# Kernel tuning notes

Measured on AMD Instinct MI355X. Metric: run time of the kernel, lower is better.

## Reference

```python
import jax, jax.numpy as jnp
import numpy as np

# Model dims (match init_kwargs / input_specs)
L = 2      # layer_dim
B = 64     # batch
T = 512    # max seq len
D = 256    # input_dim (== hidden_dim, required by stacked wiring)
H = 256    # hidden_dim
O = 2      # output_dim


def setup_inputs() -> dict:
    key = jax.random.key(0)
    ks = jax.random.split(key, 10)
    s = 1.0 / np.sqrt(H)
    f32 = jnp.float32
    return {
        "x_data": jax.random.normal(ks[0], (B, T, D), f32),
        "x_length": jax.random.randint(ks[1], (B,), 1, T + 1),
        "x_label": jax.random.uniform(ks[2], (B,), f32),
        # Per-layer GRU-cell weights, stacked over layers (bias=False).
        "Wz": (jax.random.normal(ks[3], (L, D, H), f32) * s),
        "Uz": (jax.random.normal(ks[4], (L, H, H), f32) * s),
        "Wr": (jax.random.normal(ks[5], (L, D, H), f32) * s),
        "Ur": (jax.random.normal(ks[6], (L, H, H), f32) * s),
        "Wh": (jax.random.normal(ks[7], (L, D, H), f32) * s),
        "Uh": (jax.random.normal(ks[8], (L, H, H), f32) * s),
        # Output projection of the last layer (only last layer's `out` is used).
        "Wo": (jax.random.normal(ks[9], (H, O), f32) * s),
    }


def reference(x_data, x_length, x_label, Wz, Uz, Wr, Ur, Wh, Uh, Wo):
    # Training-mode forward: sum over batch and valid timesteps of
    # (label - sigmoid(out[:, 1]))**2, with per-layer states S1, S2
    # carried across time. Vectorized over batch; lax.scan over time.
    Tn = x_data.shape[1]
    xs = jnp.swapaxes(x_data, 0, 1)  # [T, B, D]
    S1_0 = jnp.zeros((L, B, H), x_data.dtype)
    S2_0 = jnp.zeros((L, B, H), x_data.dtype)

    def step(carry, xt):
        S1, S2 = carry
        inp = xt  # [B, D]
        for l in range(L):  # small fixed layer loop
            z = jax.nn.sigmoid(inp @ Wz[l] + S1[l] @ Uz[l])
            r = jax.nn.sigmoid(inp @ Wr[l] + S1[l] @ Ur[l])
            h = jnp.tanh(inp @ Wh[l] + (r * S1[l]) @ Uh[l])
            hn = (1.0 - z) * S1[l] + z * h          # new hidden (S1)
            S2n = z * S2[l] + (1.0 - z) * h          # secondary memory (S2)
            S1 = S1.at[l].set(hn)
            S2 = S2.at[l].set(S2n)
            inp = hn
        score = jax.nn.sigmoid((inp @ Wo)[:, 1])     # out[:, 1] -> [B]
        return (S1, S2), score

    _, scores = jax.lax.scan(step, (S1_0, S2_0), xs)  # [T, B]
    mask = (jnp.arange(Tn)[:, None] < x_length[None, :]).astype(scores.dtype)
    loss = jnp.sum(mask * (x_label[None, :] - scores) ** 2)
    return loss
```

## Files before the change

kernel.cpp:

```cpp
#include <hip/hip_runtime.h>

#define LAY 2
#define BATCH 64
#define TMAX 512
#define DIM 256
#define AST 264
#define CHUNK 16

typedef float floatx4 __attribute__((ext_vector_type(4)));
typedef __bf16 bf16x8 __attribute__((ext_vector_type(8)));
#define MFMA_FP8  __builtin_amdgcn_mfma_f32_16x16x32_fp8_fp8
#define MFMA_BF16 __builtin_amdgcn_mfma_f32_16x16x32_bf16

#define BAR_LDS() asm volatile("s_waitcnt lgkmcnt(0)\n\ts_barrier" ::: "memory")

#define OFF_WPW 0x60000
#define OFF_FLG 0x150000
#define OFF_XP  0x200000
#define OFF_HP  0x1C00000
#define OFF_HN  0x3600000

__device__ __forceinline__ unsigned short f2bf(float f) {
    unsigned int u = __float_as_uint(f);
    unsigned int r = u + 0x7fffu + ((u >> 16) & 1u);
    return (unsigned short)(r >> 16);
}
__device__ __forceinline__ unsigned int pk2(float a, float b) {
    return (unsigned int)__builtin_amdgcn_cvt_pk_fp8_f32(a, b, 0, false);
}
__device__ __forceinline__ unsigned char f2q(float a) { return (unsigned char)(pk2(a, a) & 0xff); }
__device__ __forceinline__ void unp4(unsigned int u, float* f) {
    auto lo = __builtin_amdgcn_cvt_pk_f32_fp8((int)u, false);
    auto hi = __builtin_amdgcn_cvt_pk_f32_fp8((int)u, true);
    f[0] = lo[0]; f[1] = lo[1]; f[2] = hi[0]; f[3] = hi[1];
}
__device__ __forceinline__ float sigf(float x) {
    return __builtin_amdgcn_rcpf(1.f + __expf(-x));
}
__device__ __forceinline__ float tanhfast2y(float twoy) { return 2.f * sigf(twoy) - 1.f; }

__global__ void prep_weights(const float* __restrict__ Wz, const float* __restrict__ Wr,
                             const float* __restrict__ Wh, const float* __restrict__ Uz,
                             const float* __restrict__ Ur, const float* __restrict__ Uh,
                             unsigned char* __restrict__ ws, float* __restrict__ out) {
    int T = blockIdx.x * 256 + threadIdx.x;
    if (T == 0) out[0] = 0.f;
    if (T < 192) ((int*)(ws + OFF_FLG))[T] = 0;
    if (T < 196608) {
        int e = T & 3, half = (T >> 2) & 1, lane = (T >> 3) & 63;
        int kp = (T >> 9) & 3, nt = (T >> 11) & 15, mu = T >> 15;
        int g = mu % 3, l = mu / 3;
        const float* s = (g == 0 ? Uz : g == 1 ? Ur : Uh) + l * 65536;
        int n  = nt * 16 + (lane & 15);
        int k0 = (2 * kp + half) * 32 + (lane >> 4) * 8 + 2 * e;
        float w0 = s[(k0 << 8) + n] * 8.f;
        float w1 = s[((k0 + 1) << 8) + n] * 8.f;
        int addr = ((mu * 16 + nt) * 4 + kp) * 1024 + lane * 16 + half * 8 + 2 * e;
        *(unsigned short*)(ws + addr) = (unsigned short)(pk2(w0, w1) & 0xffff);
    } else {
        int T2 = T - 196608;
        int e = T2 & 3, lane = (T2 >> 2) & 63;
        int kf = (T2 >> 8) & 7, nt = (T2 >> 11) & 15, mw = T2 >> 15;
        int g = mw % 3, l = mw / 3;
        const float* s = (g == 0 ? Wz : g == 1 ? Wr : Wh) + l * 65536;
        int n  = nt * 16 + (lane & 15);
        int k0 = kf * 32 + (lane >> 4) * 8 + 2 * e;
        unsigned int v = (unsigned int)f2bf(s[(k0 << 8) + n]) |
                         ((unsigned int)f2bf(s[((k0 + 1) << 8) + n]) << 16);
        int addr = ((mw * 16 + nt) * 8 + kf) * 1024 + lane * 16 + 4 * e;
        *(unsigned int*)(ws + OFF_WPW + addr) = v;
    }
}

template <int SCORE, int WMODE, int POST>
__device__ __forceinline__ void scan_body(
    const unsigned int* __restrict__ xp, const unsigned char* __restrict__ wpU,
    int lbase, int bg, unsigned short* __restrict__ hnout,
    const int* __restrict__ xlen, const float* __restrict__ xlab,
    const float* __restrict__ Wo, float* __restrict__ out,
    int* wflags, int* pflag,
    unsigned char (*s1q)[AST], unsigned char (*rsq)[AST], float (*s1o)[264],
    float* wo1s, int* s_rdy, int tmax)
{
    const int tid = threadIdx.x, wave = tid >> 6, lane = tid & 63;
    const int l15 = lane & 15, quad = lane >> 4;
    const int b0 = bg * 16;

    for (int i = tid; i < 16 * AST; i += 1024) ((unsigned char*)s1q)[i] = 0;
    if (SCORE && tid < DIM) wo1s[tid] = Wo[2 * tid + 1];
    const int lenr = xlen[b0 + l15];
    const float labr = SCORE ? xlab[b0 + l15] : 0.f;
    (void)lenr; (void)labr;

    const int nt = wave;
    const int colA = nt * 16 + l15, rowb = quad * 4;

    long uz[8], ur[8], uh[8];
    {
        const unsigned char* pz = wpU + (size_t)(((lbase + 0) * 16 + nt) * 4) * 1024 + lane * 16;
        const unsigned char* pr = wpU + (size_t)(((lbase + 1) * 16 + nt) * 4) * 1024 + lane * 16;
        const unsigned char* ph = wpU + (size_t)(((lbase + 2) * 16 + nt) * 4) * 1024 + lane * 16;
#pragma unroll
        for (int kf = 0; kf < 8; ++kf) {
            int o = (kf >> 1) * 1024 + (kf & 1) * 8;
            uz[kf] = *(const long*)(pz + o);
            ur[kf] = *(const long*)(pr + o);
            uh[kf] = *(const long*)(ph + o);
        }
    }
    float s1r[4] = {};
    float accl = 0.f;
    int ready = 0;
    __syncthreads();

    for (int t = 0; t < tmax; ++t) {
        if constexpr (WMODE == 1) {
            if (t >= ready) {
                if (tid == 0) {
                    int vv, g = 0;
                    for (;;) {
                        vv = 1 << 30;
#pragma unroll
                        for (int q = 0; q < 4; ++q) {
                            int m = __hip_atomic_load(wflags + q, __ATOMIC_RELAXED, __HIP_MEMORY_SCOPE_AGENT);
                            vv = m < vv ? m : vv;
                        }
                        if (vv > t || ++g > (1 << 19)) break;
                        __builtin_amdgcn_s_sleep(2);
                    }
                    __threadfence();
                    *s_rdy = vv > t ? vv : t + 1;
                }
                __syncthreads();
                ready = *s_rdy;
            }
        } else if constexpr (WMODE == 2) {
            if (t >= ready) {
                if (tid == 0) {
                    const int ch = t >> 4;
                    int g = 0;
                    for (;;) {
                        int c = __hip_atomic_load(wflags + ch, __ATOMIC_RELAXED, __HIP_MEMORY_SCOPE_AGENT);
                        if (c >= 16 || ++g > (1 << 19)) break;
                        __builtin_amdgcn_s_sleep(2);
                    }
                    __threadfence();
                    *s_rdy = (ch + 1) * CHUNK;
                }
                __syncthreads();
                ready = *s_rdy;
            }
        }

        const unsigned int* xpt = xp + (size_t)(bg * 512 + t) * 3072 + lane;
        unsigned int xz = xpt[nt * 64];
        unsigned int xr = xpt[1024 + nt * 64];
        unsigned int xh = xpt[2048 + nt * 64];

        long sf[8];
#pragma unroll
        for (int kf = 0; kf < 8; ++kf) sf[kf] = *(const long*)&s1q[l15][kf * 32 + quad * 8];
        floatx4 za = {0.f, 0.f, 0.f, 0.f}, ra = za;
#pragma unroll
        for (int kf = 0; kf < 8; ++kf) {
            ra = MFMA_FP8(sf[kf], ur[kf], ra, 0, 0, 0);
            za = MFMA_FP8(sf[kf], uz[kf], za, 0, 0, 0);
        }
        float xrf[4];
        unp4(xr, xrf);
#pragma unroll
        for (int i = 0; i < 4; ++i) {
            float r = sigf(0.125f * ra[i] + 0.0625f * xrf[i]);
            rsq[rowb + i][colA] = f2q(r * s1r[i]);
        }
        BAR_LDS();

        long rf[8];
#pragma unroll
        for (int kf = 0; kf < 8; ++kf) rf[kf] = *(const long*)&rsq[l15][kf * 32 + quad * 8];
        floatx4 ha = {0.f, 0.f, 0.f, 0.f};
#pragma unroll
        for (int kf = 0; kf < 8; ++kf) ha = MFMA_FP8(rf[kf], uh[kf], ha, 0, 0, 0);
        float xzf[4], xhf[4];
        unp4(xz, xzf); unp4(xh, xhf);
#pragma unroll
        for (int i = 0; i < 4; ++i) {
            float z = sigf(0.125f * za[i] + 0.0625f * xzf[i]);
            float h = tanhfast2y(0.25f * ha[i] + 0.125f * xhf[i]);
            float hn = (1.f - z) * s1r[i] + z * h;
            s1r[i] = hn;
            s1q[rowb + i][colA] = f2q(hn);
            s1o[rowb + i][colA] = hn;
        }
        BAR_LDS();

        if (!SCORE) {
            const int r = tid >> 6, c = (tid & 63) * 4;
            float4 f0 = *(const float4*)&s1o[r][c];
            uint2 o2;
            o2.x = f2bf(f0.x) | ((unsigned)f2bf(f0.y) << 16);
            o2.y = f2bf(f0.z) | ((unsigned)f2bf(f0.w) << 16);
            *(uint2*)(hnout + ((size_t)(b0 + r) * 512 + t) * 256 + c) = o2;
        } else if (wave == 0) {
            const int row = l15, c0 = quad * 64;
            float p = 0.f;
#pragma unroll
            for (int u = 0; u < 64; u += 4) {
                float4 sv = *(const float4*)&s1o[row][c0 + u];
                float4 wv = *(const float4*)&wo1s[c0 + u];
                p = fmaf(sv.x, wv.x, p); p = fmaf(sv.y, wv.y, p);
                p = fmaf(sv.z, wv.z, p); p = fmaf(sv.w, wv.w, p);
            }
            p += __shfl_xor(p, 16);
            p += __shfl_xor(p, 32);
            if (lane < 16 && t < lenr) {
                float sc = sigf(p);
                float d = labr - sc;
                accl = fmaf(d, d, accl);
            }
        }

        if (POST && (((t & (CHUNK - 1)) == (CHUNK - 1)) || t == tmax - 1)) {
            __syncthreads();
            if (tid == 0) {
                __threadfence();
                __hip_atomic_store(pflag, t + 1, __ATOMIC_RELEASE, __HIP_MEMORY_SCOPE_AGENT);
            }
        }
    }

    if (SCORE && wave == 0) {
        accl += __shfl_xor(accl, 1);
        accl += __shfl_xor(accl, 2);
        accl += __shfl_xor(accl, 4);
        accl += __shfl_xor(accl, 8);
        if (lane == 0) atomicAdd(out, accl);
    }
}

__global__ __launch_bounds__(1024, 4) void fused_pipeline(
    const float* __restrict__ x,
    unsigned int* __restrict__ XP, unsigned int* __restrict__ HP,
    const unsigned char* __restrict__ wpU, const unsigned char* __restrict__ wpW,
    unsigned short* __restrict__ HN,
    const int* __restrict__ xlen, const float* __restrict__ xlab,
    const float* __restrict__ Wo, float* __restrict__ out, int* flags)
{
    __shared__ __align__(16) unsigned char s1q[16][AST];
    __shared__ __align__(16) unsigned char rsq[16][AST];
    __shared__ __align__(16) float s1o[16][264];
    __shared__ float wo1s[DIM];
    __shared__ int s_rdy;

    const int bid = blockIdx.x;
    const int tid = threadIdx.x, wave = tid >> 6, lane = tid & 63;
    const int l15 = lane & 15, quad = lane >> 4;
    int* cnt = flags + 32;

    if (bid >= 24) {
        const int idx = bid - 24;
        const int pt = idx & 511, pbg = idx >> 9;
        const float* s = x + ((size_t)(pbg * 16 + l15) * 512 + pt) * 256;
        bf16x8 af[8];
#pragma unroll
        for (int kf = 0; kf < 8; ++kf) {
            float4 a = *(const float4*)(s + kf * 32 + quad * 8);
            float4 b = *(const float4*)(s + kf * 32 + quad * 8 + 4);
            union { unsigned short u[8]; bf16x8 v; } cv;
            cv.u[0] = f2bf(a.x); cv.u[1] = f2bf(a.y); cv.u[2] = f2bf(a.z); cv.u[3] = f2bf(a.w);
            cv.u[4] = f2bf(b.x); cv.u[5] = f2bf(b.y); cv.u[6] = f2bf(b.z); cv.u[7] = f2bf(b.w);
            af[kf] = cv.v;
        }
        floatx4 az = {0.f, 0.f, 0.f, 0.f}, ar = az, ah = az;
        const unsigned char* bz = wpW + (size_t)((0 * 16 + wave) * 8) * 1024 + lane * 16;
        const unsigned char* br = wpW + (size_t)((1 * 16 + wave) * 8) * 1024 + lane * 16;
        const unsigned char* bh = wpW + (size_t)((2 * 16 + wave) * 8) * 1024 + lane * 16;
#pragma unroll
        for (int kf = 0; kf < 8; ++kf) {
            az = MFMA_BF16(af[kf], *(const bf16x8*)(bz + kf * 1024), az, 0, 0, 0);
            ar = MFMA_BF16(af[kf], *(const bf16x8*)(br + kf * 1024), ar, 0, 0, 0);
            ah = MFMA_BF16(af[kf], *(const bf16x8*)(bh + kf * 1024), ah, 0, 0, 0);
        }
        const size_t ob = (size_t)(pbg * 512 + pt) * 3072 + wave * 64 + lane;
        unsigned int v0 = pk2(16.f * az[0], 16.f * az[1]) | (pk2(16.f * az[2], 16.f * az[3]) << 16);
        unsigned int v1 = pk2(16.f * ar[0], 16.f * ar[1]) | (pk2(16.f * ar[2], 16.f * ar[3]) << 16);
        unsigned int v2 = pk2(16.f * ah[0], 16.f * ah[1]) | (pk2(16.f * ah[2], 16.f * ah[3]) << 16);
        __hip_atomic_store(&XP[ob],        v0, __ATOMIC_RELAXED, __HIP_MEMORY_SCOPE_AGENT);
        __hip_atomic_store(&XP[ob + 1024], v1, __ATOMIC_RELAXED, __HIP_MEMORY_SCOPE_AGENT);
        __hip_atomic_store(&XP[ob + 2048], v2, __ATOMIC_RELAXED, __HIP_MEMORY_SCOPE_AGENT);
        __syncthreads();
        if (tid == 0)
            __hip_atomic_fetch_add(cnt + pbg * 32 + (pt >> 4), 1,
                                   __ATOMIC_RELAXED, __HIP_MEMORY_SCOPE_AGENT);
        return;
    }

    int role, bg, p = 0;
    if (bid < 4)       { role = 0; bg = bid; }
    else if (bid < 20) { role = 1; bg = (bid - 4) >> 2; p = (bid - 4) & 3; }
    else               { role = 2; bg = bid - 20; }
    const int b0 = bg * 16;

    int v = xlen[b0 + l15];
#pragma unroll
    for (int o = 1; o < 16; o <<= 1) v = max(v, __shfl_xor(v, o));
    const int tmax = __builtin_amdgcn_readfirstlane(v);

    if (role == 0) {
        scan_body<0, 2, 1>(XP, wpU, 0, bg, HN, xlen, xlab, Wo, out,
                           cnt + bg * 32, flags + bg, s1q, rsq, s1o, wo1s, &s_rdy, tmax);
    } else if (role == 2) {
        scan_body<1, 1, 0>(HP, wpU, 3, bg, nullptr, xlen, xlab, Wo, out,
                           flags + 4 + bg * 4, nullptr, s1q, rsq, s1o, wo1s, &s_rdy, tmax);
    } else {
        int* wf = flags + bg;
        int* pf = flags + 4 + bg * 4 + p;
        const unsigned char* bz = wpW + (size_t)(((3 + 0) * 16 + wave) * 8) * 1024 + lane * 16;
        const unsigned char* br = wpW + (size_t)(((3 + 1) * 16 + wave) * 8) * 1024 + lane * 16;
        const unsigned char* bh = wpW + (size_t)(((3 + 2) * 16 + wave) * 8) * 1024 + lane * 16;
        for (int base = 0; base < tmax; base += CHUNK) {
            const int target = (base + CHUNK < tmax) ? base + CHUNK : tmax;
            if (tid == 0) {
                int vv, g = 0;
                for (;;) {
                    vv = __hip_atomic_load(wf, __ATOMIC_RELAXED, __HIP_MEMORY_SCOPE_AGENT);
                    if (vv >= target || ++g > (1 << 19)) break;
                    __builtin_amdgcn_s_sleep(2);
                }
                __threadfence();
            }
            __syncthreads();

            const int t0 = base + p * 4;
            const int t1 = (t0 + 4 < tmax) ? t0 + 4 : tmax;
            for (int t = t0; t < t1; ++t) {
                const unsigned short* sA = HN + ((size_t)(b0 + l15) * 512 + t) * 256;
                bf16x8 af[8];
#pragma unroll
                for (int kf = 0; kf < 8; ++kf) af[kf] = *(const bf16x8*)(sA + kf * 32 + quad * 8);
                floatx4 az = {0.f, 0.f, 0.f, 0.f}, ar = az, ah = az;
#pragma unroll
                for (int kf = 0; kf < 8; ++kf) {
                    az = MFMA_BF16(af[kf], *(const bf16x8*)(bz + kf * 1024), az, 0, 0, 0);
                    ar = MFMA_BF16(af[kf], *(const bf16x8*)(br + kf * 1024), ar, 0, 0, 0);
                    ah = MFMA_BF16(af[kf], *(const bf16x8*)(bh + kf * 1024), ah, 0, 0, 0);
                }
                const size_t ob = (size_t)(bg * 512 + t) * 3072 + wave * 64 + lane;
                HP[ob]        = pk2(16.f * az[0], 16.f * az[1]) | (pk2(16.f * az[2], 16.f * az[3]) << 16);
                HP[ob + 1024] = pk2(16.f * ar[0], 16.f * ar[1]) | (pk2(16.f * ar[2], 16.f * ar[3]) << 16);
                HP[ob + 2048] = pk2(16.f * ah[0], 16.f * ah[1]) | (pk2(16.f * ah[2], 16.f * ah[3]) << 16);
            }

            __syncthreads();
            if (tid == 0) {
                __threadfence();
                __hip_atomic_store(pf, base + CHUNK, __ATOMIC_RELEASE, __HIP_MEMORY_SCOPE_AGENT);
            }
        }
    }
}

extern "C" void kernel_launch(void* const* d_in, const int* in_sizes, int n_in,
                              void* d_out, int out_size, void* d_ws, size_t ws_size,
                              hipStream_t stream) {
    const float* x    = (const float*)d_in[0];
    const int*   xlen = (const int*)d_in[1];
    const float* xlab = (const float*)d_in[2];
    const float* Wz   = (const float*)d_in[3];
    const float* Uz   = (const float*)d_in[4];
    const float* Wr   = (const float*)d_in[5];
    const float* Ur   = (const float*)d_in[6];
    const float* Wh   = (const float*)d_in[7];
    const float* Uh   = (const float*)d_in[8];
    const float* Wo   = (const float*)d_in[9];
    float* out = (float*)d_out;

    unsigned char* ws  = (unsigned char*)d_ws;
    unsigned char* wpU = ws;
    unsigned char* wpW = ws + OFF_WPW;
    int*           FLG = (int*)(ws + OFF_FLG);
    unsigned int*  XP  = (unsigned int*)(ws + OFF_XP);
    unsigned int*  HP  = (unsigned int*)(ws + OFF_HP);
    unsigned short* HN = (unsigned short*)(ws + OFF_HN);

    prep_weights<<<1536, 256, 0, stream>>>(Wz, Wr, Wh, Uz, Ur, Uh, ws, out);
    fused_pipeline<<<2072, 1024, 0, stream>>>(x, XP, HP, wpU, wpW, HN,
                                              xlen, xlab, Wo, out, FLG);
}
```

Baseline: 1.266 ms.

## Process two batch groups per scan block to interleave independent recurrences

Each scan block now carries two 16-row batch groups (A and B) through the GRU recurrence together, sharing the register-resident U weights and interleaving independent MFMA chains and barriers. Scan blocks per layer drop from four to two, and the flag waits, score reduction and projection block dependencies are adjusted to wait on both groups. The aim is to hide MFMA and barrier latency on the serial time chain and halve barrier count per group. In exchange each step does twice the work per block, tmax becomes the max over 32 rows, and LDS use doubles.

```diff
diff --git a/kernel.cpp b/kernel.cpp
--- a/kernel.cpp
+++ b/kernel.cpp
@@ -38,6 +38,10 @@
     return __builtin_amdgcn_rcpf(1.f + __expf(-x));
 }
 __device__ __forceinline__ float tanhfast2y(float twoy) { return 2.f * sigf(twoy) - 1.f; }
+
+__device__ __forceinline__ void ast_u32(unsigned int* p, unsigned int v) {
+    __hip_atomic_store(p, v, __ATOMIC_RELAXED, __HIP_MEMORY_SCOPE_AGENT);
+}
 
 __global__ void prep_weights(const float* __restrict__ Wz, const float* __restrict__ Wr,
                              const float* __restrict__ Wh, const float* __restrict__ Uz,
@@ -73,24 +77,32 @@
 }
 
 template <int SCORE, int WMODE, int POST>
-__device__ __forceinline__ void scan_body(
+__device__ __forceinline__ void scan_pair_body(
     const unsigned int* __restrict__ xp, const unsigned char* __restrict__ wpU,
-    int lbase, int bg, unsigned short* __restrict__ hnout,
+    int lbase, int pr, unsigned short* __restrict__ hnout,
     const int* __restrict__ xlen, const float* __restrict__ xlab,
     const float* __restrict__ Wo, float* __restrict__ out,
     int* wflags, int* pflag,
-    unsigned char (*s1q)[AST], unsigned char (*rsq)[AST], float (*s1o)[264],
+    unsigned char (*s1qA)[AST], unsigned char (*s1qB)[AST],
+    unsigned char (*rsqA)[AST], unsigned char (*rsqB)[AST],
+    float (*s1oA)[264], float (*s1oB)[264],
     float* wo1s, int* s_rdy, int tmax)
 {
     const int tid = threadIdx.x, wave = tid >> 6, lane = tid & 63;
     const int l15 = lane & 15, quad = lane >> 4;
-    const int b0 = bg * 16;
-
-    for (int i = tid; i < 16 * AST; i += 1024) ((unsigned char*)s1q)[i] = 0;
+    const int bgA = 2 * pr, bgB = 2 * pr + 1;
+    const int b0A = bgA * 16, b0B = bgB * 16;
+
+    for (int i = tid; i < 16 * AST; i += 1024) {
+        ((unsigned char*)s1qA)[i] = 0;
+        ((unsigned char*)s1qB)[i] = 0;
+    }
     if (SCORE && tid < DIM) wo1s[tid] = Wo[2 * tid + 1];
-    const int lenr = xlen[b0 + l15];
-    const float labr = SCORE ? xlab[b0 + l15] : 0.f;
-    (void)lenr; (void)labr;
+    int lenr = 0; float labr = 0.f;
+    if (SCORE && wave < 2) {
+        lenr = xlen[pr * 32 + wave * 16 + l15];
+        labr = xlab[pr * 32 + wave * 16 + l15];
+    }
 
     const int nt = wave;
     const int colA = nt * 16 + l15, rowb = quad * 4;
@@ -98,17 +110,17 @@
     long uz[8], ur[8], uh[8];
     {
         const unsigned char* pz = wpU + (size_t)(((lbase + 0) * 16 + nt) * 4) * 1024 + lane * 16;
-        const unsigned char* pr = wpU + (size_t)(((lbase + 1) * 16 + nt) * 4) * 1024 + lane * 16;
+        const unsigned char* prg = wpU + (size_t)(((lbase + 1) * 16 + nt) * 4) * 1024 + lane * 16;
         const unsigned char* ph = wpU + (size_t)(((lbase + 2) * 16 + nt) * 4) * 1024 + lane * 16;
 #pragma unroll
         for (int kf = 0; kf < 8; ++kf) {
             int o = (kf >> 1) * 1024 + (kf & 1) * 8;
             uz[kf] = *(const long*)(pz + o);
-            ur[kf] = *(const long*)(pr + o);
+            ur[kf] = *(const long*)(prg + o);
             uh[kf] = *(const long*)(ph + o);
         }
     }
-    float s1r[4] = {};
+    float s1A[4] = {}, s1B[4] = {};
     float accl = 0.f;
     int ready = 0;
     __syncthreads();
@@ -121,7 +133,7 @@
                     for (;;) {
                         vv = 1 << 30;
 #pragma unroll
-                        for (int q = 0; q < 4; ++q) {
+                        for (int q = 0; q < 8; ++q) {
                             int m = __hip_atomic_load(wflags + q, __ATOMIC_RELAXED, __HIP_MEMORY_SCOPE_AGENT);
                             vv = m < vv ? m : vv;
                         }
@@ -140,8 +152,9 @@
                     const int ch = t >> 4;
                     int g = 0;
                     for (;;) {
-                        int c = __hip_atomic_load(wflags + ch, __ATOMIC_RELAXED, __HIP_MEMORY_SCOPE_AGENT);
-                        if (c >= 16 || ++g > (1 << 19)) break;
+                        int c0 = __hip_atomic_load(wflags + ch,      __ATOMIC_RELAXED, __HIP_MEMORY_SCOPE_AGENT);
+                        int c1 = __hip_atomic_load(wflags + 32 + ch, __ATOMIC_RELAXED, __HIP_MEMORY_SCOPE_AGENT);
+                        if ((c0 >= 16 && c1 >= 16) || ++g > (1 << 19)) break;
                         __builtin_amdgcn_s_sleep(2);
                     }
                     __threadfence();
@@ -152,61 +165,87 @@
             }
         }
 
-        const unsigned int* xpt = xp + (size_t)(bg * 512 + t) * 3072 + lane;
-        unsigned int xz = xpt[nt * 64];
-        unsigned int xr = xpt[1024 + nt * 64];
-        unsigned int xh = xpt[2048 + nt * 64];
-
-        long sf[8];
-#pragma unroll
-        for (int kf = 0; kf < 8; ++kf) sf[kf] = *(const long*)&s1q[l15][kf * 32 + quad * 8];
-        floatx4 za = {0.f, 0.f, 0.f, 0.f}, ra = za;
-#pragma unroll
-        for (int kf = 0; kf < 8; ++kf) {
-            ra = MFMA_FP8(sf[kf], ur[kf], ra, 0, 0, 0);
-            za = MFMA_FP8(sf[kf], uz[kf], za, 0, 0, 0);
-        }
-        float xrf[4];
-        unp4(xr, xrf);
+        const unsigned int* xptA = xp + (size_t)(bgA * 512 + t) * 3072 + lane;
+        const unsigned int* xptB = xp + (size_t)(bgB * 512 + t) * 3072 + lane;
+        unsigned int xzA = xptA[nt * 64],        xzB = xptB[nt * 64];
+        unsigned int xrA = xptA[1024 + nt * 64], xrB = xptB[1024 + nt * 64];
+        unsigned int xhA = xptA[2048 + nt * 64], xhB = xptB[2048 + nt * 64];
+
+        long sfA[8], sfB[8];
+#pragma unroll
+        for (int kf = 0; kf < 8; ++kf) {
+            sfA[kf] = *(const long*)&s1qA[l15][kf * 32 + quad * 8];
+            sfB[kf] = *(const long*)&s1qB[l15][kf * 32 + quad * 8];
+        }
+        floatx4 zer = {0.f, 0.f, 0.f, 0.f};
+        floatx4 raA = zer, raB = zer, zaA = zer, zaB = zer;
+#pragma unroll
+        for (int kf = 0; kf < 8; ++kf) {
+            raA = MFMA_FP8(sfA[kf], ur[kf], raA, 0, 0, 0);
+            raB = MFMA_FP8(sfB[kf], ur[kf], raB, 0, 0, 0);
+            zaA = MFMA_FP8(sfA[kf], uz[kf], zaA, 0, 0, 0);
+            zaB = MFMA_FP8(sfB[kf], uz[kf], zaB, 0, 0, 0);
+        }
+        float xrfA[4], xrfB[4];
+        unp4(xrA, xrfA); unp4(xrB, xrfB);
 #pragma unroll
         for (int i = 0; i < 4; ++i) {
-            float r = sigf(0.125f * ra[i] + 0.0625f * xrf[i]);
-            rsq[rowb + i][colA] = f2q(r * s1r[i]);
+            float rA = sigf(0.125f * raA[i] + 0.0625f * xrfA[i]);
+            float rB = sigf(0.125f * raB[i] + 0.0625f * xrfB[i]);
+            rsqA[rowb + i][colA] = f2q(rA * s1A[i]);
+            rsqB[rowb + i][colA] = f2q(rB * s1B[i]);
         }
         BAR_LDS();
 
-        long rf[8];
-#pragma unroll
-        for (int kf = 0; kf < 8; ++kf) rf[kf] = *(const long*)&rsq[l15][kf * 32 + quad * 8];
-        floatx4 ha = {0.f, 0.f, 0.f, 0.f};
-#pragma unroll
-        for (int kf = 0; kf < 8; ++kf) ha = MFMA_FP8(rf[kf], uh[kf], ha, 0, 0, 0);
-        float xzf[4], xhf[4];
-        unp4(xz, xzf); unp4(xh, xhf);
+        long rfA[8], rfB[8];
+#pragma unroll
+        for (int kf = 0; kf < 8; ++kf) {
+            rfA[kf] = *(const long*)&rsqA[l15][kf * 32 + quad * 8];
+            rfB[kf] = *(const long*)&rsqB[l15][kf * 32 + quad * 8];
+        }
+        floatx4 haA = zer, haB = zer;
+#pragma unroll
+        for (int kf = 0; kf < 8; ++kf) {
+            haA = MFMA_FP8(rfA[kf], uh[kf], haA, 0, 0, 0);
+            haB = MFMA_FP8(rfB[kf], uh[kf], haB, 0, 0, 0);
+        }
+        float xzfA[4], xzfB[4], xhfA[4], xhfB[4];
+        unp4(xzA, xzfA); unp4(xzB, xzfB); unp4(xhA, xhfA); unp4(xhB, xhfB);
 #pragma unroll
         for (int i = 0; i < 4; ++i) {
-            float z = sigf(0.125f * za[i] + 0.0625f * xzf[i]);
-            float h = tanhfast2y(0.25f * ha[i] + 0.125f * xhf[i]);
-            float hn = (1.f - z) * s1r[i] + z * h;
-            s1r[i] = hn;
-            s1q[rowb + i][colA] = f2q(hn);
-            s1o[rowb + i][colA] = hn;
+            float zA = sigf(0.125f * zaA[i] + 0.0625f * xzfA[i]);
+            float hA = tanhfast2y(0.25f * haA[i] + 0.125f * xhfA[i]);
+            float hnA = (1.f - zA) * s1A[i] + zA * hA;
+            s1A[i] = hnA;
+            s1qA[rowb + i][colA] = f2q(hnA);
+            s1oA[rowb + i][colA] = hnA;
+            float zB = sigf(0.125f * zaB[i] + 0.0625f * xzfB[i]);
+            float hB = tanhfast2y(0.25f * haB[i] + 0.125f * xhfB[i]);
+            float hnB = (1.f - zB) * s1B[i] + zB * hB;
+            s1B[i] = hnB;
+            s1qB[rowb + i][colA] = f2q(hnB);
+            s1oB[rowb + i][colA] = hnB;
         }
         BAR_LDS();
 
         if (!SCORE) {
             const int r = tid >> 6, c = (tid & 63) * 4;
-            float4 f0 = *(const float4*)&s1o[r][c];
-            uint2 o2;
-            o2.x = f2bf(f0.x) | ((unsigned)f2bf(f0.y) << 16);
-            o2.y = f2bf(f0.z) | ((unsigned)f2bf(f0.w) << 16);
-            *(uint2*)(hnout + ((size_t)(b0 + r) * 512 + t) * 256 + c) = o2;
-        } else if (wave == 0) {
+            float4 fa = *(const float4*)&s1oA[r][c];
+            float4 fb = *(const float4*)&s1oB[r][c];
+            uint2 oa, ob;
+            oa.x = f2bf(fa.x) | ((unsigned)f2bf(fa.y) << 16);
+            oa.y = f2bf(fa.z) | ((unsigned)f2bf(fa.w) << 16);
+            ob.x = f2bf(fb.x) | ((unsigned)f2bf(fb.y) << 16);
+            ob.y = f2bf(fb.z) | ((unsigned)f2bf(fb.w) << 16);
+            *(uint2*)(hnout + ((size_t)(b0A + r) * 512 + t) * 256 + c) = oa;
+            *(uint2*)(hnout + ((size_t)(b0B + r) * 512 + t) * 256 + c) = ob;
+        } else if (wave < 2) {
+            const float* so = (wave == 0) ? &s1oA[0][0] : &s1oB[0][0];
             const int row = l15, c0 = quad * 64;
             float p = 0.f;
 #pragma unroll
             for (int u = 0; u < 64; u += 4) {
-                float4 sv = *(const float4*)&s1o[row][c0 + u];
+                float4 sv = *(const float4*)(so + row * 264 + c0 + u);
                 float4 wv = *(const float4*)&wo1s[c0 + u];
                 p = fmaf(sv.x, wv.x, p); p = fmaf(sv.y, wv.y, p);
                 p = fmaf(sv.z, wv.z, p); p = fmaf(sv.w, wv.w, p);
@@ -229,7 +268,7 @@
         }
     }
 
-    if (SCORE && wave == 0) {
+    if (SCORE && wave < 2) {
         accl += __shfl_xor(accl, 1);
         accl += __shfl_xor(accl, 2);
         accl += __shfl_xor(accl, 4);
@@ -246,9 +285,12 @@
     const int* __restrict__ xlen, const float* __restrict__ xlab,
     const float* __restrict__ Wo, float* __restrict__ out, int* flags)
 {
-    __shared__ __align__(16) unsigned char s1q[16][AST];
-    __shared__ __align__(16) unsigned char rsq[16][AST];
-    __shared__ __align__(16) float s1o[16][264];
+    __shared__ __align__(16) unsigned char s1qA[16][AST];
+    __shared__ __align__(16) unsigned char s1qB[16][AST];
+    __shared__ __align__(16) unsigned char rsqA[16][AST];
+    __shared__ __align__(16) unsigned char rsqB[16][AST];
+    __shared__ __align__(16) float s1oA[16][264];
+    __shared__ __align__(16) float s1oB[16][264];
     __shared__ float wo1s[DIM];
     __shared__ int s_rdy;
 
@@ -257,8 +299,8 @@
     const int l15 = lane & 15, quad = lane >> 4;
     int* cnt = flags + 32;
 
-    if (bid >= 24) {
-        const int idx = bid - 24;
+    if (bid >= 20) {
+        const int idx = bid - 20;
         const int pt = idx & 511, pbg = idx >> 9;
         const float* s = x + ((size_t)(pbg * 16 + l15) * 512 + pt) * 256;
         bf16x8 af[8];
@@ -282,12 +324,9 @@
             ah = MFMA_BF16(af[kf], *(const bf16x8*)(bh + kf * 1024), ah, 0, 0, 0);
         }
         const size_t ob = (size_t)(pbg * 512 + pt) * 3072 + wave * 64 + lane;
-        unsigned int v0 = pk2(16.f * az[0], 16.f * az[1]) | (pk2(16.f * az[2], 16.f * az[3]) << 16);
-        unsigned int v1 = pk2(16.f * ar[0], 16.f * ar[1]) | (pk2(16.f * ar[2], 16.f * ar[3]) << 16);
-        unsigned int v2 = pk2(16.f * ah[0], 16.f * ah[1]) | (pk2(16.f * ah[2], 16.f * ah[3]) << 16);
-        __hip_atomic_store(&XP[ob],        v0, __ATOMIC_RELAXED, __HIP_MEMORY_SCOPE_AGENT);
-        __hip_atomic_store(&XP[ob + 1024], v1, __ATOMIC_RELAXED, __HIP_MEMORY_SCOPE_AGENT);
-        __hip_atomic_store(&XP[ob + 2048], v2, __ATOMIC_RELAXED, __HIP_MEMORY_SCOPE_AGENT);
+        ast_u32(&XP[ob],        pk2(16.f * az[0], 16.f * az[1]) | (pk2(16.f * az[2], 16.f * az[3]) << 16));
+        ast_u32(&XP[ob + 1024], pk2(16.f * ar[0], 16.f * ar[1]) | (pk2(16.f * ar[2], 16.f * ar[3]) << 16));
+        ast_u32(&XP[ob + 2048], pk2(16.f * ah[0], 16.f * ah[1]) | (pk2(16.f * ah[2], 16.f * ah[3]) << 16));
         __syncthreads();
         if (tid == 0)
             __hip_atomic_fetch_add(cnt + pbg * 32 + (pt >> 4), 1,
@@ -295,67 +334,85 @@
         return;
     }
 
-    int role, bg, p = 0;
-    if (bid < 4)       { role = 0; bg = bid; }
-    else if (bid < 20) { role = 1; bg = (bid - 4) >> 2; p = (bid - 4) & 3; }
-    else               { role = 2; bg = bid - 20; }
+    int role, pr = 0, bg = 0, p = 0;
+    if (bid < 2)       { role = 0; pr = bid; }
+    else if (bid < 18) { role = 1; bg = (bid - 2) >> 2; p = (bid - 2) & 3; }
+    else               { role = 2; pr = bid - 18; }
+
+    if (role == 0 || role == 2) {
+        int v = max(xlen[pr * 32 + l15], xlen[pr * 32 + 16 + l15]);
+#pragma unroll
+        for (int o = 1; o < 16; o <<= 1) v = max(v, __shfl_xor(v, o));
+        const int tmax = __builtin_amdgcn_readfirstlane(v);
+
+        if (role == 0) {
+            scan_pair_body<0, 2, 1>(XP, wpU, 0, pr, HN, xlen, xlab, Wo, out,
+                                    cnt + pr * 64, flags + pr,
+                                    s1qA, s1qB, rsqA, rsqB, s1oA, s1oB,
+                                    wo1s, &s_rdy, tmax);
+        } else {
+            scan_pair_body<1, 1, 0>(HP, wpU, 3, pr, nullptr, xlen, xlab, Wo, out,
+                                    flags + 4 + pr * 8, nullptr,
+                                    s1qA, s1qB, rsqA, rsqB, s1oA, s1oB,
+                                    wo1s, &s_rdy, tmax);
+        }
+        return;
+    }
+
     const int b0 = bg * 16;
-
     int v = xlen[b0 + l15];
 #pragma unroll
     for (int o = 1; o < 16; o <<= 1) v = max(v, __shfl_xor(v, o));
-    const int tmax = __builtin_amdgcn_readfirstlane(v);
-
-    if (role == 0) {
-        scan_body<0, 2, 1>(XP, wpU, 0, bg, HN, xlen, xlab, Wo, out,
-                           cnt + bg * 32, flags + bg, s1q, rsq, s1o, wo1s, &s_rdy, tmax);
-    } else if (role == 2) {
-        scan_body<1, 1, 0>(HP, wpU, 3, bg, nullptr, xlen, xlab, Wo, out,
-                           flags + 4 + bg * 4, nullptr, s1q, rsq, s1o, wo1s, &s_rdy, tmax);
-    } else {
-        int* wf = flags + bg;
-        int* pf = flags + 4 + bg * 4 + p;
-        const unsigned char* bz = wpW + (size_t)(((3 + 0) * 16 + wave) * 8) * 1024 + lane * 16;
-        const unsigned char* br = wpW + (size_t)(((3 + 1) * 16 + wave) * 8) * 1024 + lane * 16;
-        const unsigned char* bh = wpW + (size_t)(((3 + 2) * 16 + wave) * 8) * 1024 + lane * 16;
-        for (int base = 0; base < tmax; base += CHUNK) {
-            const int target = (base + CHUNK < tmax) ? base + CHUNK : tmax;
-            if (tid == 0) {
-                int vv, g = 0;
-                for (;;) {
-                    vv = __hip_atomic_load(wf, __ATOMIC_RELAXED, __HIP_MEMORY_SCOPE_AGENT);
-                    if (vv >= target || ++g > (1 << 19)) break;
-                    __builtin_amdgcn_s_sleep(2);
-                }
-                __threadfence();
-            }
-            __syncthreads();
-
-            const int t0 = base + p * 4;
-            const int t1 = (t0 + 4 < tmax) ? t0 + 4 : tmax;
-            for (int t = t0; t < t1; ++t) {
-                const unsigned short* sA = HN + ((size_t)(b0 + l15) * 512 + t) * 256;
-                bf16x8 af[8];
-#pragma unroll
-                for (int kf = 0; kf < 8; ++kf) af[kf] = *(const bf16x8*)(sA + kf * 32 + quad * 8);
-                floatx4 az = {0.f, 0.f, 0.f, 0.f}, ar = az, ah = az;
-#pragma unroll
-                for (int kf = 0; kf < 8; ++kf) {
-                    az = MFMA_BF16(af[kf], *(const bf16x8*)(bz + kf * 1024), az, 0, 0, 0);
-                    ar = MFMA_BF16(af[kf], *(const bf16x8*)(br + kf * 1024), ar, 0, 0, 0);
-                    ah = MFMA_BF16(af[kf], *(const bf16x8*)(bh + kf * 1024), ah, 0, 0, 0);
-                }
-                const size_t ob = (size_t)(bg * 512 + t) * 3072 + wave * 64 + lane;
-                HP[ob]        = pk2(16.f * az[0], 16.f * az[1]) | (pk2(16.f * az[2], 16.f * az[3]) << 16);
-                HP[ob + 1024] = pk2(16.f * ar[0], 16.f * ar[1]) | (pk2(16.f * ar[2], 16.f * ar[3]) << 16);
-                HP[ob + 2048] = pk2(16.f * ah[0], 16.f * ah[1]) | (pk2(16.f * ah[2], 16.f * ah[3]) << 16);
-            }
-
-            __syncthreads();
-            if (tid == 0) {
-                __threadfence();
-                __hip_atomic_store(pf, base + CHUNK, __ATOMIC_RELEASE, __HIP_MEMORY_SCOPE_AGENT);
-            }
+    int tmax = __builtin_amdgcn_readfirstlane(v);
+    {
+        int v2 = xlen[(bg ^ 1) * 16 + l15];
+#pragma unroll
+        for (int o = 1; o < 16; o <<= 1) v2 = max(v2, __shfl_xor(v2, o));
+        int tm2 = __builtin_amdgcn_readfirstlane(v2);
+        tmax = max(tmax, tm2);
+    }
+    int* wf = flags + (bg >> 1);
+    int* pf = flags + 4 + bg * 4 + p;
+    const unsigned char* bz = wpW + (size_t)(((3 + 0) * 16 + wave) * 8) * 1024 + lane * 16;
+    const unsigned char* br = wpW + (size_t)(((3 + 1) * 16 + wave) * 8) * 1024 + lane * 16;
+    const unsigned char* bh = wpW + (size_t)(((3 + 2) * 16 + wave) * 8) * 1024 + lane * 16;
+    for (int base = 0; base < tmax; base += CHUNK) {
+        const int target = (base + CHUNK < tmax) ? base + CHUNK : tmax;
+        if (tid == 0) {
+            int vv, g = 0;
+            for (;;) {
+                vv = __hip_atomic_load(wf, __ATOMIC_RELAXED, __HIP_MEMORY_SCOPE_AGENT);
+                if (vv >= target || ++g > (1 << 19)) break;
+                __builtin_amdgcn_s_sleep(2);
+            }
+            __threadfence();
+        }
+        __syncthreads();
+
+        const int t0 = base + p * 4;
+        const int t1 = (t0 + 4 < tmax) ? t0 + 4 : tmax;
+        for (int t = t0; t < t1; ++t) {
+            const unsigned short* sA = HN + ((size_t)(b0 + l15) * 512 + t) * 256;
+            bf16x8 af[8];
+#pragma unroll
+            for (int kf = 0; kf < 8; ++kf) af[kf] = *(const bf16x8*)(sA + kf * 32 + quad * 8);
+            floatx4 az = {0.f, 0.f, 0.f, 0.f}, ar = az, ah = az;
+#pragma unroll
+            for (int kf = 0; kf < 8; ++kf) {
+                az = MFMA_BF16(af[kf], *(const bf16x8*)(bz + kf * 1024), az, 0, 0, 0);
+                ar = MFMA_BF16(af[kf], *(const bf16x8*)(br + kf * 1024), ar, 0, 0, 0);
+                ah = MFMA_BF16(af[kf], *(const bf16x8*)(bh + kf * 1024), ah, 0, 0, 0);
+            }
+            const size_t ob = (size_t)(bg * 512 + t) * 3072 + wave * 64 + lane;
+            HP[ob]        = pk2(16.f * az[0], 16.f * az[1]) | (pk2(16.f * az[2], 16.f * az[3]) << 16);
+            HP[ob + 1024] = pk2(16.f * ar[0], 16.f * ar[1]) | (pk2(16.f * ar[2], 16.f * ar[3]) << 16);
+            HP[ob + 2048] = pk2(16.f * ah[0], 16.f * ah[1]) | (pk2(16.f * ah[2], 16.f * ah[3]) << 16);
+        }
+
+        __syncthreads();
+        if (tid == 0) {
+            __threadfence();
+            __hip_atomic_store(pf, base + CHUNK, __ATOMIC_RELEASE, __HIP_MEMORY_SCOPE_AGENT);
         }
     }
 }
@@ -384,6 +441,6 @@
     unsigned short* HN = (unsigned short*)(ws + OFF_HN);
 
     prep_weights<<<1536, 256, 0, stream>>>(Wz, Wr, Wh, Uz, Ur, Uh, ws, out);
-    fused_pipeline<<<2072, 1024, 0, stream>>>(x, XP, HP, wpU, wpW, HN,
+    fused_pipeline<<<2068, 1024, 0, stream>>>(x, XP, HP, wpU, wpW, HN,
                                               xlen, xlab, Wo, out, FLG);
 }
```

New measurement: 2.180 ms. 1.72x slower.
